# Kernel tuning notes

Hardware: AMD Instinct MI355X
Metric: run time of the kernel (lower is better)

## Reference

```python
import jax, jax.numpy as jnp
import numpy as np

B, S, DIN, DQK, DV = 4, 4096, 1024, 64, 64


def setup_inputs() -> dict:
    key = jax.random.key(0)
    ks = jax.random.split(key, 10)
    inv = 1.0 / np.sqrt(DIN)
    return {
        "query": jax.random.normal(ks[0], (B, S, DIN), dtype=jnp.float32),
        "key": jax.random.normal(ks[1], (B, S, DIN), dtype=jnp.float32),
        "value": jax.random.normal(ks[2], (B, S, DIN), dtype=jnp.float32),
        "mask": jnp.ones((B, S, S), dtype=jnp.int32),
        "Wq": jax.random.uniform(ks[3], (DIN, DQK), jnp.float32, -inv, inv),
        "bq": jax.random.uniform(ks[4], (DQK,), jnp.float32, -inv, inv),
        "Wk": jax.random.uniform(ks[5], (DIN, DQK), jnp.float32, -inv, inv),
        "bk": jax.random.uniform(ks[6], (DQK,), jnp.float32, -inv, inv),
        "Wv": jax.random.uniform(ks[7], (DIN, DV), jnp.float32, -inv, inv),
        "bv": jax.random.uniform(ks[8], (DV,), jnp.float32, -inv, inv),
    }


def reference(query, key, value, mask, Wq, bq, Wk, bk, Wv, bv):
    q = jnp.einsum("bsd,de->bse", query, Wq) + bq  # [B,S,DQK]
    k = jnp.einsum("bsd,de->bse", key, Wk) + bk    # [B,S,DQK]
    v = jnp.einsum("bsd,de->bse", value, Wv) + bv  # [B,S,DV]
    # faithful nonstandard scale: sqrt(dim_qk + 1e-8)
    scale = jnp.sqrt(jnp.float32(q.shape[-1]) + 1e-8)
    scores = jnp.einsum("bqe,bke->bqk", q, k) / scale  # [B,S,S]
    scores = jnp.where(mask == 0, jnp.float32(-jnp.inf), scores)
    attn = jax.nn.softmax(scores, axis=-1)
    return jnp.einsum("bqk,bkv->bqv", attn, v)  # [B,S,DV]
```

## Files before the change

kernel.cpp:

```cpp
#include <hip/hip_runtime.h>

#define NB 4
#define NS 4096
#define NDIN 1024
#define ND 64

typedef __attribute__((ext_vector_type(4))) float f32x4;
typedef __attribute__((ext_vector_type(8))) short s16x8;
typedef __attribute__((ext_vector_type(4))) short s16x4;

__device__ __forceinline__ unsigned short f2bf(float f) {
  union { float f; unsigned u; } x; x.f = f;
  unsigned r = x.u + 0x7fffu + ((x.u >> 16) & 1u);
  return (unsigned short)(r >> 16);
}

__device__ __forceinline__ unsigned cvtpk(float lo, float hi) {
  unsigned r;
  asm("v_cvt_pk_bf16_f32 %0, %1, %2" : "=v"(r) : "v"(lo), "v"(hi));
  return r;
}

__device__ __forceinline__ void gload16(const void* g, void* l) {
  __builtin_amdgcn_global_load_lds(
      (const __attribute__((address_space(1))) void*)g,
      (__attribute__((address_space(3))) void*)l, 16, 0, 0);
}

__global__ __launch_bounds__(256) void prep_w_kernel(
    const float* __restrict__ Wq, const float* __restrict__ Wk,
    const float* __restrict__ Wv, unsigned short* __restrict__ wt) {
  int idx = blockIdx.x * 256 + threadIdx.x;
  int m = idx >> 16;
  int r = idx & 65535;
  int c = r >> 10;
  int k = r & 1023;
  const float* W = (m == 0) ? Wq : (m == 1) ? Wk : Wv;
  wt[idx] = f2bf(W[k * ND + c]);
}

__global__ __launch_bounds__(256, 3) void proj_kernel(
    const float* __restrict__ Xq, const float* __restrict__ Xk, const float* __restrict__ Xv,
    const float* __restrict__ bq, const float* __restrict__ bk, const float* __restrict__ bv,
    const unsigned short* __restrict__ wt_all,
    unsigned short* __restrict__ q_o, unsigned short* __restrict__ k_o,
    unsigned short* __restrict__ vt_o) {
  __shared__ float xsm[2][4096];
  __shared__ unsigned short wsm[2][4096];

  const int y = blockIdx.y;
  const float* __restrict__ X = (y == 0) ? Xq : (y == 1) ? Xk : Xv;
  const float* __restrict__ bias = (y == 0) ? bq : (y == 1) ? bk : bv;
  const char* __restrict__ wg = (const char*)(wt_all + y * (ND * NDIN));
  const int row0 = blockIdx.x * 64;
  const int tid = threadIdx.x;
  const int lane = tid & 63;
  const int w = tid >> 6;
  const int ql = lane & 15;
  const int grp = lane >> 4;
  const int swz = (ql & 7) << 4;

  int osrcX[4];
  #pragma unroll
  for (int j = 0; j < 4; ++j) {
    const int o = w * 4096 + j * 1024 + lane * 16;
    const int row = o >> 8, c = o & 255;
    osrcX[j] = row * 4096 + (c ^ ((row & 7) << 4));
  }
  int osrcW[2];
  #pragma unroll
  for (int j = 0; j < 2; ++j) {
    const int o = w * 2048 + j * 1024 + lane * 16;
    const int row = o >> 7, c = o & 127;
    osrcW[j] = row * 2048 + (c ^ ((row & 7) << 4));
  }

  const char* xg = (const char*)(X + (size_t)row0 * NDIN);
  auto stageX = [&](int kk, int buf) {
    const char* src = xg + kk * 256;
    char* dst = (char*)xsm + buf * 16384 + w * 4096;
    #pragma unroll
    for (int j = 0; j < 4; ++j) gload16(src + osrcX[j], dst + j * 1024);
  };
  auto stageW = [&](int kk, int buf) {
    const char* src = wg + kk * 128;
    char* dst = (char*)wsm + buf * 8192 + w * 2048;
    gload16(src + osrcW[0], dst);
    gload16(src + osrcW[1], dst + 1024);
  };

  const int fw0 = (grp * 16) ^ swz;
  const int fw1 = (grp * 16 + 64) ^ swz;

  f32x4 acc[4] = {};

  stageX(0, 0);
  stageW(0, 0);
  asm volatile("s_waitcnt vmcnt(0)" ::: "memory");
  __syncthreads();

  for (int kk = 0; kk < 16; ++kk) {
    const int cur = kk & 1;
    if (kk < 15) {
      stageX(kk + 1, cur ^ 1);
      stageW(kk + 1, cur ^ 1);
    }
    __builtin_amdgcn_sched_barrier(0);

    const char* xr = (const char*)xsm + cur * 16384 + (16 * w + ql) * 256;
    const char* wr = (const char*)wsm + cur * 8192;
    #pragma unroll
    for (int half = 0; half < 2; ++half) {
      const f32x4 a0 = *reinterpret_cast<const f32x4*>(
          xr + ((half * 128 + grp * 32) ^ swz));
      const f32x4 a1 = *reinterpret_cast<const f32x4*>(
          xr + ((half * 128 + grp * 32 + 16) ^ swz));
      union { s16x8 v; unsigned u[4]; } a;
      a.u[0] = cvtpk(a0[0], a0[1]);
      a.u[1] = cvtpk(a0[2], a0[3]);
      a.u[2] = cvtpk(a1[0], a1[1]);
      a.u[3] = cvtpk(a1[2], a1[3]);
      const int fw = half ? fw1 : fw0;
      #pragma unroll
      for (int nt = 0; nt < 4; ++nt) {
        const s16x8 bfr = *reinterpret_cast<const s16x8*>(wr + (ql + 16 * nt) * 128 + fw);
        acc[nt] = __builtin_amdgcn_mfma_f32_16x16x32_bf16(a.v, bfr, acc[nt], 0, 0, 0);
      }
    }

    asm volatile("s_waitcnt vmcnt(0)" ::: "memory");
    __syncthreads();
  }

  const int b = row0 >> 12;
  const int s0 = row0 & 4095;
  #pragma unroll
  for (int nt = 0; nt < 4; ++nt) {
    const int col = ql + 16 * nt;
    const float bia = bias[col];
    #pragma unroll
    for (int r = 0; r < 4; ++r) {
      const int rr = 16 * w + grp * 4 + r;
      const unsigned short h = f2bf(acc[nt][r] + bia);
      if (y == 0) {
        q_o[(size_t)(row0 + rr) * ND + col] = h;
      } else if (y == 1) {
        k_o[(size_t)(row0 + rr) * ND + col] = h;
      } else {
        vt_o[(size_t)b * ND * NS + (size_t)col * NS + (s0 + rr)] = h;
      }
    }
  }
}

__global__ __launch_bounds__(256, 4) void attn_kernel(
    const unsigned short* __restrict__ qm, const unsigned short* __restrict__ km,
    const unsigned short* __restrict__ vt, const int* __restrict__ mask,
    float* __restrict__ opart, float* __restrict__ ml) {
  __shared__ unsigned short ksm[2][4096];
  __shared__ unsigned short vsm[2][4096];
  __shared__ unsigned short psm[4096];

  const int bid = blockIdx.x;
  const int combo = bid & 15;
  const int qblk = bid >> 4;
  const int b = combo >> 2;
  const int split = combo & 3;
  const int q0 = qblk * 64;
  const int kv00 = split * 1024;

  const int tid = threadIdx.x;
  const int lane = tid & 63;
  const int w = tid >> 6;
  const int ql = lane & 15;
  const int grp = lane >> 4;

  const int swz = (ql & 7) << 4;
  const int fK0 = ql * 128 + ((grp * 16) ^ swz);
  const int fK1 = ql * 128 + ((grp * 16 + 64) ^ swz);

  int oK0, oK1, oV0, oV1;
  {
    const int o0 = w * 2048 + lane * 16;
    const int o1 = o0 + 1024;
    oK0 = o0 ^ (((o0 >> 7) & 7) << 4);
    oK1 = o1 ^ (((o1 >> 7) & 7) << 4);
    const int d0 = o0 >> 7, c0 = o0 & 127;
    const int d1 = o1 >> 7, c1 = o1 & 127;
    oV0 = d0 * 8192 + (c0 ^ ((d0 & 7) << 4));
    oV1 = d1 * 8192 + (c1 ^ ((d1 & 7) << 4));
  }

  const char* kg = (const char*)(km + (size_t)b * NS * ND + (size_t)kv00 * ND);
  const char* vg = (const char*)(vt + (size_t)b * ND * NS + kv00);
  char* const klds = (char*)&ksm[0][0] + w * 2048;
  char* const vlds = (char*)&vsm[0][0] + w * 2048;
  char* const pw = (char*)&psm[0] + w * 2048;

  const size_t qrow = (size_t)(b * NS + q0 + w * 16 + ql) * ND;
  const s16x8 qf0 = *reinterpret_cast<const s16x8*>(qm + qrow + grp * 8);
  const s16x8 qf1 = *reinterpret_cast<const s16x8*>(qm + qrow + 32 + grp * 8);

  const int* __restrict__ mrow =
      mask + (size_t)(b * NS + q0 + w * 16 + ql) * NS + kv00;

  f32x4 acc[4] = {};
  float m_i = -INFINITY;
  float l_i = 0.f;
  const float CSC = 0.18033688011112042f;
  const float THR = 11.54f;

  auto stage = [&](int t, int buf) {
    const char* kt = kg + (size_t)t * 8192;
    const char* vtb = vg + (size_t)t * 128;
    gload16(kt + oK0, klds + buf * 8192);
    gload16(kt + oK1, klds + buf * 8192 + 1024);
    gload16(vtb + oV0, vlds + buf * 8192);
    gload16(vtb + oV1, vlds + buf * 8192 + 1024);
  };

  int4 mc[2][4];

  stage(0, 0);
  {
    mc[0][0] = *reinterpret_cast<const int4*>(mrow + grp * 4);
    mc[0][1] = *reinterpret_cast<const int4*>(mrow + 16 + grp * 4);
    mc[0][2] = *reinterpret_cast<const int4*>(mrow + 32 + grp * 4);
    mc[0][3] = *reinterpret_cast<const int4*>(mrow + 48 + grp * 4);
  }
  asm volatile("s_waitcnt vmcnt(0)" ::: "memory");
  __syncthreads();

  for (int tt = 0; tt < 16; tt += 2) {
    #pragma unroll
    for (int ph = 0; ph < 2; ++ph) {
      const int t = tt + ph;
      const int cur = ph;

      if (t < 15) {
        stage(t + 1, cur ^ 1);
        __builtin_amdgcn_sched_barrier(0);
        const int* mn = mrow + (t + 1) * 64;
        mc[ph ^ 1][0] = *reinterpret_cast<const int4*>(mn + grp * 4);
        mc[ph ^ 1][1] = *reinterpret_cast<const int4*>(mn + 16 + grp * 4);
        mc[ph ^ 1][2] = *reinterpret_cast<const int4*>(mn + 32 + grp * 4);
        mc[ph ^ 1][3] = *reinterpret_cast<const int4*>(mn + 48 + grp * 4);
      }
      __builtin_amdgcn_sched_barrier(0);

      const char* kread = (const char*)&ksm[0][0] + cur * 8192;
      const char* vread = (const char*)&vsm[0][0] + cur * 8192;

      f32x4 s4[4];
      __builtin_amdgcn_s_setprio(1);
      #pragma unroll
      for (int mt = 0; mt < 4; ++mt) {
        const s16x8 kf0 = *reinterpret_cast<const s16x8*>(kread + mt * 2048 + fK0);
        const s16x8 kf1 = *reinterpret_cast<const s16x8*>(kread + mt * 2048 + fK1);
        f32x4 s = {0.f, 0.f, 0.f, 0.f};
        s = __builtin_amdgcn_mfma_f32_16x16x32_bf16(kf0, qf0, s, 0, 0, 0);
        s = __builtin_amdgcn_mfma_f32_16x16x32_bf16(kf1, qf1, s, 0, 0, 0);
        s4[mt] = s;
      }
      __builtin_amdgcn_s_setprio(0);

      float sc[16];
      #pragma unroll
      for (int mt = 0; mt < 4; ++mt) {
        const int4 m = mc[ph][mt];
        sc[4 * mt + 0] = (m.x != 0) ? s4[mt][0] * CSC : -1e30f;
        sc[4 * mt + 1] = (m.y != 0) ? s4[mt][1] * CSC : -1e30f;
        sc[4 * mt + 2] = (m.z != 0) ? s4[mt][2] * CSC : -1e30f;
        sc[4 * mt + 3] = (m.w != 0) ? s4[mt][3] * CSC : -1e30f;
      }

      float t0 = fmaxf(fmaxf(sc[0], sc[1]), fmaxf(sc[2], sc[3]));
      float t1 = fmaxf(fmaxf(sc[4], sc[5]), fmaxf(sc[6], sc[7]));
      float t2 = fmaxf(fmaxf(sc[8], sc[9]), fmaxf(sc[10], sc[11]));
      float t3 = fmaxf(fmaxf(sc[12], sc[13]), fmaxf(sc[14], sc[15]));
      float tm = fmaxf(fmaxf(t0, t1), fmaxf(t2, t3));
      tm = fmaxf(tm, __shfl_xor(tm, 16));
      tm = fmaxf(tm, __shfl_xor(tm, 32));
      if (!__all(tm <= m_i + THR)) {
        const float nm = fmaxf(m_i, tm);
        const float alpha = exp2f(m_i - nm);
        #pragma unroll
        for (int r = 0; r < 4; ++r) {
          const float ar = __shfl(alpha, grp * 4 + r);
          acc[0][r] *= ar;
          acc[1][r] *= ar;
          acc[2][r] *= ar;
          acc[3][r] *= ar;
        }
        l_i *= alpha;
        m_i = nm;
      }
      #pragma unroll
      for (int r = 0; r < 16; ++r) sc[r] = exp2f(sc[r] - m_i);
      float u0 = (sc[0] + sc[1]) + (sc[2] + sc[3]);
      float u1 = (sc[4] + sc[5]) + (sc[6] + sc[7]);
      float u2 = (sc[8] + sc[9]) + (sc[10] + sc[11]);
      float u3 = (sc[12] + sc[13]) + (sc[14] + sc[15]);
      float ssum = (u0 + u1) + (u2 + u3);
      ssum += __shfl_xor(ssum, 16);
      ssum += __shfl_xor(ssum, 32);
      l_i += ssum;

      #pragma unroll
      for (int mt = 0; mt < 4; ++mt) {
        uint2 pk;
        pk.x = cvtpk(sc[4 * mt + 0], sc[4 * mt + 1]);
        pk.y = cvtpk(sc[4 * mt + 2], sc[4 * mt + 3]);
        *reinterpret_cast<uint2*>(pw + ql * 128 + ((mt * 32 + grp * 8) ^ swz)) = pk;
      }

      #pragma unroll
      for (int ks = 0; ks < 2; ++ks) {
        const s16x8 pa = *reinterpret_cast<const s16x8*>(
            pw + ql * 128 + ((ks * 64 + grp * 16) ^ swz));
        const int fV = ks ? fK1 : fK0;
        __builtin_amdgcn_s_setprio(1);
        #pragma unroll
        for (int nt = 0; nt < 4; ++nt) {
          const s16x8 vb = *reinterpret_cast<const s16x8*>(vread + nt * 2048 + fV);
          acc[nt] = __builtin_amdgcn_mfma_f32_16x16x32_bf16(pa, vb, acc[nt], 0, 0, 0);
        }
        __builtin_amdgcn_s_setprio(0);
      }

      if (t < 15) {
        asm volatile("s_waitcnt vmcnt(4)" ::: "memory");
        __builtin_amdgcn_s_barrier();
      }
    }
  }

  const int qg = b * NS + q0 + w * 16;
  float* obase = opart + ((size_t)split * (NB * NS) + qg) * 64;
  #pragma unroll
  for (int nt = 0; nt < 4; ++nt) {
    #pragma unroll
    for (int r = 0; r < 4; ++r) {
      obase[(size_t)(grp * 4 + r) * 64 + ql + 16 * nt] = acc[nt][r];
    }
  }
  if (grp == 0) {
    float* mlp = ml + ((size_t)split * (NB * NS) + qg + ql) * 2;
    mlp[0] = m_i;
    mlp[1] = l_i;
  }
}

__global__ __launch_bounds__(256) void combine_kernel(
    const float* __restrict__ opart, const float* __restrict__ ml,
    float* __restrict__ out) {
  const int idx = blockIdx.x * 256 + threadIdx.x;
  const int q = idx >> 4;
  const int dc = (idx & 15) * 4;
  const float2 a0 = *reinterpret_cast<const float2*>(ml + (size_t)q * 2);
  const float2 a1 = *reinterpret_cast<const float2*>(ml + (size_t)(16384 + q) * 2);
  const float2 a2 = *reinterpret_cast<const float2*>(ml + (size_t)(32768 + q) * 2);
  const float2 a3 = *reinterpret_cast<const float2*>(ml + (size_t)(49152 + q) * 2);
  const float M = fmaxf(fmaxf(a0.x, a1.x), fmaxf(a2.x, a3.x));
  const float w0 = exp2f(a0.x - M), w1 = exp2f(a1.x - M);
  const float w2 = exp2f(a2.x - M), w3 = exp2f(a3.x - M);
  const float inv = 1.f / (a0.y * w0 + a1.y * w1 + a2.y * w2 + a3.y * w3);
  f32x4 o = (*reinterpret_cast<const f32x4*>(opart + (size_t)q * 64 + dc)) * w0;
  o += (*reinterpret_cast<const f32x4*>(opart + ((size_t)16384 + q) * 64 + dc)) * w1;
  o += (*reinterpret_cast<const f32x4*>(opart + ((size_t)32768 + q) * 64 + dc)) * w2;
  o += (*reinterpret_cast<const f32x4*>(opart + ((size_t)49152 + q) * 64 + dc)) * w3;
  o *= inv;
  *reinterpret_cast<f32x4*>(out + (size_t)q * 64 + dc) = o;
}

extern "C" void kernel_launch(void* const* d_in, const int* in_sizes, int n_in,
                              void* d_out, int out_size, void* d_ws, size_t ws_size,
                              hipStream_t stream) {
  const float* query = (const float*)d_in[0];
  const float* key   = (const float*)d_in[1];
  const float* value = (const float*)d_in[2];
  const int*   mask  = (const int*)d_in[3];
  const float* Wq = (const float*)d_in[4];
  const float* bq = (const float*)d_in[5];
  const float* Wk = (const float*)d_in[6];
  const float* bk = (const float*)d_in[7];
  const float* Wv = (const float*)d_in[8];
  const float* bv = (const float*)d_in[9];
  float* out = (float*)d_out;

  char* ws = (char*)d_ws;
  unsigned short* wt    = (unsigned short*)(ws);
  unsigned short* qb    = (unsigned short*)(ws + 393216);
  unsigned short* kb    = (unsigned short*)(ws + 2490368);
  unsigned short* vtb   = (unsigned short*)(ws + 4587520);
  float*          opart = (float*)(ws + 6684672);
  float*          mlb   = (float*)(ws + 23461888);

  prep_w_kernel<<<dim3(768), dim3(256), 0, stream>>>(Wq, Wk, Wv, wt);
  proj_kernel<<<dim3(256, 3), dim3(256), 0, stream>>>(query, key, value,
                                                      bq, bk, bv, wt, qb, kb, vtb);
  attn_kernel<<<dim3(1024), dim3(256), 0, stream>>>(qb, kb, vtb, mask, opart, mlb);
  combine_kernel<<<dim3(1024), dim3(256), 0, stream>>>(opart, mlb, out);
}
```

Before: 130.9 us.

## Pack int32 mask into bitmask in a prepass and defer row-sum reductions

Adds a separate kernel that turns the int32 attention mask into one bit per element. The attention kernel then loads a single 64-bit word per tile instead of four int4 vectors, and its wait counter drops from 4 to 1. The attention loop now skips the cross-lane max shuffles unless a lane needs a rescale, and it reduces the row sum l only once after the loop. The full mask is still read once, now in a standalone streaming pass instead of overlapped with attention compute, so the extra launch and lost overlap may cancel the savings.

```diff
diff --git a/kernel.cpp b/kernel.cpp
--- a/kernel.cpp
+++ b/kernel.cpp
@@ -37,6 +37,19 @@
   int k = r & 1023;
   const float* W = (m == 0) ? Wq : (m == 1) ? Wk : Wv;
   wt[idx] = f2bf(W[k * ND + c]);
+}
+
+__global__ __launch_bounds__(256) void mask_pack_kernel(
+    const int* __restrict__ mask, unsigned char* __restrict__ bits) {
+  const int idx = blockIdx.x * 256 + threadIdx.x;
+  const int4* mp = reinterpret_cast<const int4*>(mask) + (size_t)idx * 2;
+  const int4 a = mp[0];
+  const int4 c = mp[1];
+  unsigned v = (unsigned)(a.x != 0) | ((unsigned)(a.y != 0) << 1) |
+               ((unsigned)(a.z != 0) << 2) | ((unsigned)(a.w != 0) << 3) |
+               ((unsigned)(c.x != 0) << 4) | ((unsigned)(c.y != 0) << 5) |
+               ((unsigned)(c.z != 0) << 6) | ((unsigned)(c.w != 0) << 7);
+  bits[idx] = (unsigned char)v;
 }
 
 __global__ __launch_bounds__(256, 3) void proj_kernel(
@@ -155,7 +168,7 @@
 
 __global__ __launch_bounds__(256, 4) void attn_kernel(
     const unsigned short* __restrict__ qm, const unsigned short* __restrict__ km,
-    const unsigned short* __restrict__ vt, const int* __restrict__ mask,
+    const unsigned short* __restrict__ vt, const unsigned char* __restrict__ mbits,
     float* __restrict__ opart, float* __restrict__ ml) {
   __shared__ unsigned short ksm[2][4096];
   __shared__ unsigned short vsm[2][4096];
@@ -201,8 +214,8 @@
   const s16x8 qf0 = *reinterpret_cast<const s16x8*>(qm + qrow + grp * 8);
   const s16x8 qf1 = *reinterpret_cast<const s16x8*>(qm + qrow + 32 + grp * 8);
 
-  const int* __restrict__ mrow =
-      mask + (size_t)(b * NS + q0 + w * 16 + ql) * NS + kv00;
+  const unsigned char* __restrict__ mrow8 =
+      mbits + (size_t)(b * NS + q0 + w * 16 + ql) * (NS / 8) + split * 128;
 
   f32x4 acc[4] = {};
   float m_i = -INFINITY;
@@ -219,121 +232,113 @@
     gload16(vtb + oV1, vlds + buf * 8192 + 1024);
   };
 
-  int4 mc[2][4];
-
+  auto body = [&](int t, const char* kread, const char* vread, int buf_next,
+                  unsigned long long mbc, unsigned long long& mbn) {
+    if (t < 15) {
+      stage(t + 1, buf_next);
+      __builtin_amdgcn_sched_barrier(0);
+      mbn = *reinterpret_cast<const unsigned long long*>(mrow8 + (t + 1) * 8);
+    }
+    __builtin_amdgcn_sched_barrier(0);
+
+    f32x4 s4[4];
+    __builtin_amdgcn_s_setprio(1);
+    #pragma unroll
+    for (int mt = 0; mt < 4; ++mt) {
+      const s16x8 kf0 = *reinterpret_cast<const s16x8*>(kread + mt * 2048 + fK0);
+      const s16x8 kf1 = *reinterpret_cast<const s16x8*>(kread + mt * 2048 + fK1);
+      f32x4 s = {0.f, 0.f, 0.f, 0.f};
+      s = __builtin_amdgcn_mfma_f32_16x16x32_bf16(kf0, qf0, s, 0, 0, 0);
+      s = __builtin_amdgcn_mfma_f32_16x16x32_bf16(kf1, qf1, s, 0, 0, 0);
+      s4[mt] = s;
+    }
+    __builtin_amdgcn_s_setprio(0);
+
+    float sc[16];
+    #pragma unroll
+    for (int mt = 0; mt < 4; ++mt) {
+      const unsigned nib = (unsigned)((mbc >> (16 * mt + 4 * grp)) & 0xFull);
+      sc[4 * mt + 0] = (nib & 1u) ? s4[mt][0] * CSC : -1e30f;
+      sc[4 * mt + 1] = (nib & 2u) ? s4[mt][1] * CSC : -1e30f;
+      sc[4 * mt + 2] = (nib & 4u) ? s4[mt][2] * CSC : -1e30f;
+      sc[4 * mt + 3] = (nib & 8u) ? s4[mt][3] * CSC : -1e30f;
+    }
+
+    float t0 = fmaxf(fmaxf(sc[0], sc[1]), fmaxf(sc[2], sc[3]));
+    float t1 = fmaxf(fmaxf(sc[4], sc[5]), fmaxf(sc[6], sc[7]));
+    float t2 = fmaxf(fmaxf(sc[8], sc[9]), fmaxf(sc[10], sc[11]));
+    float t3 = fmaxf(fmaxf(sc[12], sc[13]), fmaxf(sc[14], sc[15]));
+    const float tm = fmaxf(fmaxf(t0, t1), fmaxf(t2, t3));
+    if (!__all(tm <= m_i + THR)) {
+      float tw = fmaxf(tm, __shfl_xor(tm, 16));
+      tw = fmaxf(tw, __shfl_xor(tw, 32));
+      const float nm = fmaxf(m_i, tw);
+      const float alpha = exp2f(m_i - nm);
+      #pragma unroll
+      for (int r = 0; r < 4; ++r) {
+        const float ar = __shfl(alpha, grp * 4 + r);
+        acc[0][r] *= ar;
+        acc[1][r] *= ar;
+        acc[2][r] *= ar;
+        acc[3][r] *= ar;
+      }
+      l_i *= alpha;
+      m_i = nm;
+    }
+    #pragma unroll
+    for (int r = 0; r < 16; ++r) sc[r] = exp2f(sc[r] - m_i);
+    float u0 = (sc[0] + sc[1]) + (sc[2] + sc[3]);
+    float u1 = (sc[4] + sc[5]) + (sc[6] + sc[7]);
+    float u2 = (sc[8] + sc[9]) + (sc[10] + sc[11]);
+    float u3 = (sc[12] + sc[13]) + (sc[14] + sc[15]);
+    l_i += (u0 + u1) + (u2 + u3);
+
+    #pragma unroll
+    for (int mt = 0; mt < 4; ++mt) {
+      uint2 pk;
+      pk.x = cvtpk(sc[4 * mt + 0], sc[4 * mt + 1]);
+      pk.y = cvtpk(sc[4 * mt + 2], sc[4 * mt + 3]);
+      *reinterpret_cast<uint2*>(pw + ql * 128 + ((mt * 32 + grp * 8) ^ swz)) = pk;
+    }
+
+    #pragma unroll
+    for (int ks = 0; ks < 2; ++ks) {
+      const s16x8 pa = *reinterpret_cast<const s16x8*>(
+          pw + ql * 128 + ((ks * 64 + grp * 16) ^ swz));
+      const int fV = ks ? fK1 : fK0;
+      __builtin_amdgcn_s_setprio(1);
+      #pragma unroll
+      for (int nt = 0; nt < 4; ++nt) {
+        const s16x8 vb = *reinterpret_cast<const s16x8*>(vread + nt * 2048 + fV);
+        acc[nt] = __builtin_amdgcn_mfma_f32_16x16x32_bf16(pa, vb, acc[nt], 0, 0, 0);
+      }
+      __builtin_amdgcn_s_setprio(0);
+    }
+
+    if (t < 15) {
+      asm volatile("s_waitcnt vmcnt(1)" ::: "memory");
+      __builtin_amdgcn_s_barrier();
+    }
+  };
+
+  const char* const kbuf0 = (const char*)&ksm[0][0];
+  const char* const kbuf1 = (const char*)&ksm[0][0] + 8192;
+  const char* const vbuf0 = (const char*)&vsm[0][0];
+  const char* const vbuf1 = (const char*)&vsm[0][0] + 8192;
+
+  unsigned long long mbA, mbB;
   stage(0, 0);
-  {
-    mc[0][0] = *reinterpret_cast<const int4*>(mrow + grp * 4);
-    mc[0][1] = *reinterpret_cast<const int4*>(mrow + 16 + grp * 4);
-    mc[0][2] = *reinterpret_cast<const int4*>(mrow + 32 + grp * 4);
-    mc[0][3] = *reinterpret_cast<const int4*>(mrow + 48 + grp * 4);
-  }
+  mbA = *reinterpret_cast<const unsigned long long*>(mrow8);
   asm volatile("s_waitcnt vmcnt(0)" ::: "memory");
   __syncthreads();
 
   for (int tt = 0; tt < 16; tt += 2) {
-    #pragma unroll
-    for (int ph = 0; ph < 2; ++ph) {
-      const int t = tt + ph;
-      const int cur = ph;
-
-      if (t < 15) {
-        stage(t + 1, cur ^ 1);
-        __builtin_amdgcn_sched_barrier(0);
-        const int* mn = mrow + (t + 1) * 64;
-        mc[ph ^ 1][0] = *reinterpret_cast<const int4*>(mn + grp * 4);
-        mc[ph ^ 1][1] = *reinterpret_cast<const int4*>(mn + 16 + grp * 4);
-        mc[ph ^ 1][2] = *reinterpret_cast<const int4*>(mn + 32 + grp * 4);
-        mc[ph ^ 1][3] = *reinterpret_cast<const int4*>(mn + 48 + grp * 4);
-      }
-      __builtin_amdgcn_sched_barrier(0);
-
-      const char* kread = (const char*)&ksm[0][0] + cur * 8192;
-      const char* vread = (const char*)&vsm[0][0] + cur * 8192;
-
-      f32x4 s4[4];
-      __builtin_amdgcn_s_setprio(1);
-      #pragma unroll
-      for (int mt = 0; mt < 4; ++mt) {
-        const s16x8 kf0 = *reinterpret_cast<const s16x8*>(kread + mt * 2048 + fK0);
-        const s16x8 kf1 = *reinterpret_cast<const s16x8*>(kread + mt * 2048 + fK1);
-        f32x4 s = {0.f, 0.f, 0.f, 0.f};
-        s = __builtin_amdgcn_mfma_f32_16x16x32_bf16(kf0, qf0, s, 0, 0, 0);
-        s = __builtin_amdgcn_mfma_f32_16x16x32_bf16(kf1, qf1, s, 0, 0, 0);
-        s4[mt] = s;
-      }
-      __builtin_amdgcn_s_setprio(0);
-
-      float sc[16];
-      #pragma unroll
-      for (int mt = 0; mt < 4; ++mt) {
-        const int4 m = mc[ph][mt];
-        sc[4 * mt + 0] = (m.x != 0) ? s4[mt][0] * CSC : -1e30f;
-        sc[4 * mt + 1] = (m.y != 0) ? s4[mt][1] * CSC : -1e30f;
-        sc[4 * mt + 2] = (m.z != 0) ? s4[mt][2] * CSC : -1e30f;
-        sc[4 * mt + 3] = (m.w != 0) ? s4[mt][3] * CSC : -1e30f;
-      }
-
-      float t0 = fmaxf(fmaxf(sc[0], sc[1]), fmaxf(sc[2], sc[3]));
-      float t1 = fmaxf(fmaxf(sc[4], sc[5]), fmaxf(sc[6], sc[7]));
-      float t2 = fmaxf(fmaxf(sc[8], sc[9]), fmaxf(sc[10], sc[11]));
-      float t3 = fmaxf(fmaxf(sc[12], sc[13]), fmaxf(sc[14], sc[15]));
-      float tm = fmaxf(fmaxf(t0, t1), fmaxf(t2, t3));
-      tm = fmaxf(tm, __shfl_xor(tm, 16));
-      tm = fmaxf(tm, __shfl_xor(tm, 32));
-      if (!__all(tm <= m_i + THR)) {
-        const float nm = fmaxf(m_i, tm);
-        const float alpha = exp2f(m_i - nm);
-        #pragma unroll
-        for (int r = 0; r < 4; ++r) {
-          const float ar = __shfl(alpha, grp * 4 + r);
-          acc[0][r] *= ar;
-          acc[1][r] *= ar;
-          acc[2][r] *= ar;
-          acc[3][r] *= ar;
-        }
-        l_i *= alpha;
-        m_i = nm;
-      }
-      #pragma unroll
-      for (int r = 0; r < 16; ++r) sc[r] = exp2f(sc[r] - m_i);
-      float u0 = (sc[0] + sc[1]) + (sc[2] + sc[3]);
-      float u1 = (sc[4] + sc[5]) + (sc[6] + sc[7]);
-      float u2 = (sc[8] + sc[9]) + (sc[10] + sc[11]);
-      float u3 = (sc[12] + sc[13]) + (sc[14] + sc[15]);
-      float ssum = (u0 + u1) + (u2 + u3);
-      ssum += __shfl_xor(ssum, 16);
-      ssum += __shfl_xor(ssum, 32);
-      l_i += ssum;
-
-      #pragma unroll
-      for (int mt = 0; mt < 4; ++mt) {
-        uint2 pk;
-        pk.x = cvtpk(sc[4 * mt + 0], sc[4 * mt + 1]);
-        pk.y = cvtpk(sc[4 * mt + 2], sc[4 * mt + 3]);
-        *reinterpret_cast<uint2*>(pw + ql * 128 + ((mt * 32 + grp * 8) ^ swz)) = pk;
-      }
-
-      #pragma unroll
-      for (int ks = 0; ks < 2; ++ks) {
-        const s16x8 pa = *reinterpret_cast<const s16x8*>(
-            pw + ql * 128 + ((ks * 64 + grp * 16) ^ swz));
-        const int fV = ks ? fK1 : fK0;
-        __builtin_amdgcn_s_setprio(1);
-        #pragma unroll
-        for (int nt = 0; nt < 4; ++nt) {
-          const s16x8 vb = *reinterpret_cast<const s16x8*>(vread + nt * 2048 + fV);
-          acc[nt] = __builtin_amdgcn_mfma_f32_16x16x32_bf16(pa, vb, acc[nt], 0, 0, 0);
-        }
-        __builtin_amdgcn_s_setprio(0);
-      }
-
-      if (t < 15) {
-        asm volatile("s_waitcnt vmcnt(4)" ::: "memory");
-        __builtin_amdgcn_s_barrier();
-      }
-    }
-  }
+    body(tt, kbuf0, vbuf0, 1, mbA, mbB);
+    body(tt + 1, kbuf1, vbuf1, 0, mbB, mbA);
+  }
+
+  float lq = l_i + __shfl_xor(l_i, 16);
+  lq += __shfl_xor(lq, 32);
 
   const int qg = b * NS + q0 + w * 16;
   float* obase = opart + ((size_t)split * (NB * NS) + qg) * 64;
@@ -347,7 +352,7 @@
   if (grp == 0) {
     float* mlp = ml + ((size_t)split * (NB * NS) + qg + ql) * 2;
     mlp[0] = m_i;
-    mlp[1] = l_i;
+    mlp[1] = lq;
   }
 }
 
@@ -393,12 +398,14 @@
   unsigned short* qb    = (unsigned short*)(ws + 393216);
   unsigned short* kb    = (unsigned short*)(ws + 2490368);
   unsigned short* vtb   = (unsigned short*)(ws + 4587520);
-  float*          opart = (float*)(ws + 6684672);
-  float*          mlb   = (float*)(ws + 23461888);
+  unsigned char*  mbits = (unsigned char*)(ws + 6684672);
+  float*          opart = (float*)(ws + 15073280);
+  float*          mlb   = (float*)(ws + 31850496);
 
   prep_w_kernel<<<dim3(768), dim3(256), 0, stream>>>(Wq, Wk, Wv, wt);
+  mask_pack_kernel<<<dim3(32768), dim3(256), 0, stream>>>(mask, mbits);
   proj_kernel<<<dim3(256, 3), dim3(256), 0, stream>>>(query, key, value,
                                                       bq, bk, bv, wt, qb, kb, vtb);
-  attn_kernel<<<dim3(1024), dim3(256), 0, stream>>>(qb, kb, vtb, mask, opart, mlb);
+  attn_kernel<<<dim3(1024), dim3(256), 0, stream>>>(qb, kb, vtb, mbits, opart, mlb);
   combine_kernel<<<dim3(1024), dim3(256), 0, stream>>>(opart, mlb, out);
 }
```

Result: slower. 143.3 us (+9.5%).
